# Kernel tuning notes

Hardware: AMD Instinct MI355X
Metric: run time of the kernel (lower is better)

Reference implementation:

```python
import jax, jax.numpy as jnp
import numpy as np

N_NODES = 20000
N_EDGES = 320000
IN_DIM = 128
HID = 64
HEADS = 4
NEG_SLOPE = 0.2  # PyG GATConv default


def _glorot(key, shape):
    fan_in, fan_out = shape[0], shape[-1]
    lim = jnp.sqrt(6.0 / (fan_in + fan_out))
    return jax.random.uniform(key, shape, jnp.float32, -lim, lim)


def setup_inputs() -> dict:
    key = jax.random.key(0)
    ks = jax.random.split(key, 16)
    x = jax.random.normal(ks[0], (N_NODES, IN_DIM), jnp.float32)
    edge_index = jax.random.randint(ks[1], (2, N_EDGES), 0, N_NODES, dtype=jnp.int64)
    # layer 1: in=128 -> heads=4, out=64, concat
    W1 = _glorot(ks[2], (IN_DIM, HEADS * HID))
    a_src1 = _glorot(ks[3], (HEADS, HID))
    a_dst1 = _glorot(ks[4], (HEADS, HID))
    b1 = jnp.zeros((HEADS * HID,), jnp.float32)
    # layer 2: in=256 -> heads=4, out=64, concat
    W2 = _glorot(ks[5], (HEADS * HID, HEADS * HID))
    a_src2 = _glorot(ks[6], (HEADS, HID))
    a_dst2 = _glorot(ks[7], (HEADS, HID))
    b2 = jnp.zeros((HEADS * HID,), jnp.float32)
    # layer 3: in=256 -> heads=1, out=1, mean (concat=False)
    W3 = _glorot(ks[8], (HEADS * HID, 1))
    a_src3 = _glorot(ks[9], (1, 1))
    a_dst3 = _glorot(ks[10], (1, 1))
    b3 = jnp.zeros((1,), jnp.float32)
    return {
        "x": x, "edge_index": edge_index,
        "W1": W1, "a_src1": a_src1, "a_dst1": a_dst1, "b1": b1,
        "W2": W2, "a_src2": a_src2, "a_dst2": a_dst2, "b2": b2,
        "W3": W3, "a_src3": a_src3, "a_dst3": a_dst3, "b3": b3,
    }


def gat_conv(x, src, dst, W, a_src, a_dst, b, heads, out_c, concat):
    """PyG GATConv (add_self_loops already applied to src/dst)."""
    n = x.shape[0]
    h = (x @ W).reshape(n, heads, out_c)            # [N,H,C]
    alpha_s = jnp.sum(h * a_src, axis=-1)           # [N,H]
    alpha_d = jnp.sum(h * a_dst, axis=-1)           # [N,H]
    e = jax.nn.leaky_relu(alpha_s[src] + alpha_d[dst], NEG_SLOPE)  # [E,H]
    # segment softmax over incoming edges of each destination node
    e_max = jax.ops.segment_max(e, dst, num_segments=n)            # [N,H]
    ex = jnp.exp(e - e_max[dst])                                   # [E,H]
    denom = jax.ops.segment_sum(ex, dst, num_segments=n)           # [N,H]
    alpha = ex / denom[dst]                                        # [E,H]
    msg = h[src] * alpha[:, :, None]                               # [E,H,C]
    out = jax.ops.segment_sum(msg, dst, num_segments=n)            # [N,H,C]
    if concat:
        out = out.reshape(n, heads * out_c)
    else:
        out = out.mean(axis=1)
    return out + b


def reference(x, edge_index, W1, a_src1, a_dst1, b1, W2, a_src2, a_dst2, b2,
              W3, a_src3, a_dst3, b3):
    n = x.shape[0]
    loops = jnp.arange(n, dtype=edge_index.dtype)
    src = jnp.concatenate([edge_index[0], loops])
    dst = jnp.concatenate([edge_index[1], loops])
    h = jax.nn.elu(gat_conv(x, src, dst, W1, a_src1, a_dst1, b1, HEADS, HID, True))
    # dropout is identity in eval mode
    h = jax.nn.elu(gat_conv(h, src, dst, W2, a_src2, a_dst2, b2, HEADS, HID, True))
    h = gat_conv(h, src, dst, W3, a_src3, a_dst3, b3, 1, 1, False)
    return h.reshape(-1)
```

## Files before the change

kernel.cpp:

```cpp
#include <hip/hip_runtime.h>
#include <hip/hip_bf16.h>
#include <cmath>

#define N_NODESC 20000
#define E_RAW    320000
#define E_TOTC   340000
#define HEADSC   4
#define FC       256
#define NEG_SLOPE 0.2f
#define MAXD     512

typedef __attribute__((ext_vector_type(8))) short short8v;
typedef __attribute__((ext_vector_type(4))) float f32x4;

__device__ __forceinline__ int dstOf(const int* ei, int e) {
  return (e < E_RAW) ? ei[E_RAW + e] : (e - E_RAW);
}
__device__ __forceinline__ int srcOf(const int* ei, int e) {
  return (e < E_RAW) ? ei[e] : (e - E_RAW);
}
__device__ __forceinline__ float lrelu(float v) { return v > 0.f ? v : NEG_SLOPE * v; }

__device__ __forceinline__ unsigned short f2bf(float f) {
  __hip_bfloat16 h = __float2bfloat16(f);
  return reinterpret_cast<unsigned short&>(h);
}
__device__ __forceinline__ float bf2f(unsigned short u) {
  return __uint_as_float(((unsigned int)u) << 16);
}

__global__ void mega_prep(const float* __restrict__ x,
                          unsigned short* __restrict__ xhi, unsigned short* __restrict__ xlo,
                          const float* __restrict__ W1,
                          unsigned short* __restrict__ w1hi, unsigned short* __restrict__ w1lo,
                          const float* __restrict__ W2,
                          unsigned short* __restrict__ w2hi, unsigned short* __restrict__ w2lo,
                          int* __restrict__ deg) {
  const int bid = blockIdx.x, t = threadIdx.x;
  if (bid < 10000) {
    int i = bid * 256 + t;
    float v = x[i];
    unsigned short hh = f2bf(v);
    xhi[i] = hh; xlo[i] = f2bf(v - bf2f(hh));
  } else if (bid < 10128) {
    int idx = (bid - 10000) * 256 + t;
    int c = idx >> 7, k = idx & 127;
    float v = W1[k * FC + c];
    unsigned short hh = f2bf(v);
    w1hi[c * 128 + k] = hh; w1lo[c * 128 + k] = f2bf(v - bf2f(hh));
  } else if (bid < 10384) {
    int idx = (bid - 10128) * 256 + t;
    int c = idx >> 8, k = idx & 255;
    float v = W2[k * FC + c];
    unsigned short hh = f2bf(v);
    w2hi[c * 256 + k] = hh; w2lo[c * 256 + k] = f2bf(v - bf2f(hh));
  } else {
    int i = (bid - 10384) * 256 + t;
    if (i < N_NODESC) deg[i] = 0;
  }
}

template<int K>
__global__ void __launch_bounds__(256) mfma_gemm(
    const unsigned short* __restrict__ Ahi, const unsigned short* __restrict__ Alo,
    const unsigned short* __restrict__ WhiT, const unsigned short* __restrict__ WloT,
    const float* __restrict__ a_src, const float* __restrict__ a_dst,
    unsigned short* __restrict__ hb, float* __restrict__ as, float* __restrict__ ad) {
  __shared__ float asred[64][4];
  __shared__ float adred[64][4];
  const int t = threadIdx.x;
  const int w = t >> 6, l = t & 63;
  const int n0 = blockIdx.x * 64;
  const int r16 = l & 15;
  const int kq = l >> 4;
  const int col0 = w * 64;

  f32x4 acc[4][4];
#pragma unroll
  for (int rt = 0; rt < 4; ++rt)
#pragma unroll
    for (int ct = 0; ct < 4; ++ct) acc[rt][ct] = f32x4{0.f, 0.f, 0.f, 0.f};

  long arow[4];
#pragma unroll
  for (int rt = 0; rt < 4; ++rt) {
    int r = n0 + rt * 16 + r16;
    if (r >= N_NODESC) r = N_NODESC - 1;
    arow[rt] = (long)r * K;
  }

  for (int ks = 0; ks < K; ks += 32) {
    const int kb = ks + kq * 8;
    short8v aHi[4], aLo[4];
#pragma unroll
    for (int rt = 0; rt < 4; ++rt) {
      aHi[rt] = *(const short8v*)(Ahi + arow[rt] + kb);
      aLo[rt] = *(const short8v*)(Alo + arow[rt] + kb);
    }
#pragma unroll
    for (int ct = 0; ct < 4; ++ct) {
      const long wrow = (long)(col0 + ct * 16 + r16) * K + kb;
      short8v wHi = *(const short8v*)(WhiT + wrow);
      short8v wLo = *(const short8v*)(WloT + wrow);
#pragma unroll
      for (int rt = 0; rt < 4; ++rt) {
        acc[rt][ct] = __builtin_amdgcn_mfma_f32_16x16x32_bf16(aHi[rt], wHi, acc[rt][ct], 0, 0, 0);
        acc[rt][ct] = __builtin_amdgcn_mfma_f32_16x16x32_bf16(aHi[rt], wLo, acc[rt][ct], 0, 0, 0);
        acc[rt][ct] = __builtin_amdgcn_mfma_f32_16x16x32_bf16(aLo[rt], wHi, acc[rt][ct], 0, 0, 0);
      }
    }
  }

  float asv[4], adv[4];
#pragma unroll
  for (int ct = 0; ct < 4; ++ct) {
    int c = col0 + ct * 16 + r16;
    asv[ct] = a_src[c];
    adv[ct] = a_dst[c];
  }
#pragma unroll
  for (int rt = 0; rt < 4; ++rt) {
#pragma unroll
    for (int j = 0; j < 4; ++j) {
      const int r = rt * 16 + kq * 4 + j;
      const int g = n0 + r;
      if (g < N_NODESC) {
#pragma unroll
        for (int ct = 0; ct < 4; ++ct)
          hb[(long)g * FC + col0 + ct * 16 + r16] = f2bf(acc[rt][ct][j]);
      }
      float ps = acc[rt][0][j] * asv[0] + acc[rt][1][j] * asv[1]
               + acc[rt][2][j] * asv[2] + acc[rt][3][j] * asv[3];
      float pd = acc[rt][0][j] * adv[0] + acc[rt][1][j] * adv[1]
               + acc[rt][2][j] * adv[2] + acc[rt][3][j] * adv[3];
      for (int off = 8; off; off >>= 1) {
        ps += __shfl_down(ps, off, 16);
        pd += __shfl_down(pd, off, 16);
      }
      if (r16 == 0) {
        asred[r][w] = ps;
        adred[r][w] = pd;
      }
    }
  }
  __syncthreads();
  {
    const int rr = t >> 2, hh = t & 3;
    const int g = n0 + rr;
    if (g < N_NODESC) {
      as[(long)g * HEADSC + hh] = asred[rr][hh];
      ad[(long)g * HEADSC + hh] = adred[rr][hh];
    }
  }
}

__global__ void deg_count(const int* __restrict__ ei, int* __restrict__ deg) {
  int e = blockIdx.x * 256 + threadIdx.x;
  if (e >= E_TOTC) return;
  atomicAdd(&deg[dstOf(ei, e)], 1);
}

__global__ void scan_kernel(const int* __restrict__ deg, int* __restrict__ row_ptr,
                            int* __restrict__ cursor) {
  const int t = threadIdx.x;
  const int lane = t & 63, wid = t >> 6;
  const int PER = (N_NODESC + 1023) / 1024;
  const int base = t * PER;
  int own = 0;
  for (int i = 0; i < PER; ++i) {
    int idx = base + i;
    if (idx < N_NODESC) own += deg[idx];
  }
  int inc = own;
  for (int off = 1; off < 64; off <<= 1) {
    int v = __shfl_up(inc, off, 64);
    if (lane >= off) inc += v;
  }
  __shared__ int wtot[16], woff[16];
  if (lane == 63) wtot[wid] = inc;
  __syncthreads();
  if (t == 0) {
    int r = 0;
    for (int i = 0; i < 16; ++i) { woff[i] = r; r += wtot[i]; }
  }
  __syncthreads();
  int run = woff[wid] + inc - own;
  for (int i = 0; i < PER; ++i) {
    int idx = base + i;
    if (idx < N_NODESC) {
      row_ptr[idx] = run;
      cursor[idx]  = run;
      run += deg[idx];
    }
  }
  if (t == 1023) row_ptr[N_NODESC] = run;
}

__global__ void fill_kernel(const int* __restrict__ ei, int* __restrict__ cursor,
                            int* __restrict__ col_src) {
  int e = blockIdx.x * 256 + threadIdx.x;
  if (e >= E_TOTC) return;
  int d = dstOf(ei, e);
  int pos = atomicAdd(&cursor[d], 1);
  col_src[pos] = srcOf(ei, e);
}

template<int MODE>
__global__ void __launch_bounds__(128) fused_sa(
    const int* __restrict__ row_ptr, const int* __restrict__ col_src,
    const float4* __restrict__ as4, const float4* __restrict__ ad4,
    const unsigned short* __restrict__ hb, const float* __restrict__ b,
    unsigned short* __restrict__ out_hi, unsigned short* __restrict__ out_lo,
    const float* __restrict__ W3, const float* __restrict__ asc3,
    const float* __restrict__ adc3, float* __restrict__ h3,
    float* __restrict__ a3s, float* __restrict__ a3d) {
  const int d = blockIdx.x;
  const int t = threadIdx.x;
  const int l = t & 63, wv = t >> 6;
  const int j0 = row_ptr[d], j1 = row_ptr[d + 1];
  const int deg = j1 - j0;
  __shared__ float4 wbuf[MAXD];
  __shared__ float4 xred[2];
  const float4 adv = ad4[d];

  float4 mx = float4{-INFINITY, -INFINITY, -INFINITY, -INFINITY};
  for (int j = j0 + t; j < j1; j += 128) {
    float4 a = as4[col_src[j]];
    float4 v;
    v.x = lrelu(a.x + adv.x); v.y = lrelu(a.y + adv.y);
    v.z = lrelu(a.z + adv.z); v.w = lrelu(a.w + adv.w);
    int jj = j - j0;
    if (jj < MAXD) wbuf[jj] = v;
    mx.x = fmaxf(mx.x, v.x); mx.y = fmaxf(mx.y, v.y);
    mx.z = fmaxf(mx.z, v.z); mx.w = fmaxf(mx.w, v.w);
  }
  for (int off = 32; off; off >>= 1) {
    mx.x = fmaxf(mx.x, __shfl_xor(mx.x, off, 64));
    mx.y = fmaxf(mx.y, __shfl_xor(mx.y, off, 64));
    mx.z = fmaxf(mx.z, __shfl_xor(mx.z, off, 64));
    mx.w = fmaxf(mx.w, __shfl_xor(mx.w, off, 64));
  }
  if (l == 0) xred[wv] = mx;
  __syncthreads();
  {
    float4 m0 = xred[0], m1 = xred[1];
    mx.x = fmaxf(m0.x, m1.x); mx.y = fmaxf(m0.y, m1.y);
    mx.z = fmaxf(m0.z, m1.z); mx.w = fmaxf(m0.w, m1.w);
  }
  __syncthreads();

  float4 sm = float4{0.f, 0.f, 0.f, 0.f};
  for (int j = j0 + t; j < j1; j += 128) {
    int jj = j - j0;
    float4 v;
    if (jj < MAXD) v = wbuf[jj];
    else {
      float4 a = as4[col_src[j]];
      v.x = lrelu(a.x + adv.x); v.y = lrelu(a.y + adv.y);
      v.z = lrelu(a.z + adv.z); v.w = lrelu(a.w + adv.w);
    }
    float4 e;
    e.x = expf(v.x - mx.x); e.y = expf(v.y - mx.y);
    e.z = expf(v.z - mx.z); e.w = expf(v.w - mx.w);
    if (jj < MAXD) wbuf[jj] = e;
    sm.x += e.x; sm.y += e.y; sm.z += e.z; sm.w += e.w;
  }
  for (int off = 32; off; off >>= 1) {
    sm.x += __shfl_xor(sm.x, off, 64);
    sm.y += __shfl_xor(sm.y, off, 64);
    sm.z += __shfl_xor(sm.z, off, 64);
    sm.w += __shfl_xor(sm.w, off, 64);
  }
  if (l == 0) xred[wv] = sm;
  __syncthreads();

  const int h = t >> 5;
  float st0, mxh, advh;
  {
    float4 s0 = xred[0], s1 = xred[1];
    float sx = s0.x + s1.x, sy = s0.y + s1.y, sz = s0.z + s1.z, sw = s0.w + s1.w;
    st0  = (h == 0) ? sx : (h == 1) ? sy : (h == 2) ? sz : sw;
    mxh  = (h == 0) ? mx.x : (h == 1) ? mx.y : (h == 2) ? mx.z : mx.w;
    advh = (h == 0) ? adv.x : (h == 1) ? adv.y : (h == 2) ? adv.z : adv.w;
  }
  const float dnh = 1.f / st0;

  const float* wlds = (const float*)wbuf;
  const ushort2* hb2 = (const ushort2*)hb;
  float a0 = 0.f, a1 = 0.f;
  if (deg <= MAXD) {
    int j = j0;
    for (; j + 8 <= j1; j += 8) {
      int     s[8];
      ushort2 v[8];
      float   w[8];
#pragma unroll
      for (int u = 0; u < 8; ++u) s[u] = col_src[j + u];
#pragma unroll
      for (int u = 0; u < 8; ++u) v[u] = hb2[(long)s[u] * 128 + t];
#pragma unroll
      for (int u = 0; u < 8; ++u) w[u] = wlds[(j + u - j0) * 4 + h];
#pragma unroll
      for (int u = 0; u < 8; ++u) {
        a0 = fmaf(w[u], bf2f(v[u].x), a0);
        a1 = fmaf(w[u], bf2f(v[u].y), a1);
      }
    }
    for (; j < j1; ++j) {
      ushort2 v = hb2[(long)col_src[j] * 128 + t];
      float w = wlds[(j - j0) * 4 + h];
      a0 = fmaf(w, bf2f(v.x), a0);
      a1 = fmaf(w, bf2f(v.y), a1);
    }
  } else {
    const float* asf = (const float*)as4;
    for (int j = j0; j < j1; ++j) {
      int s = col_src[j];
      float e = expf(lrelu(asf[s * 4 + h] + advh) - mxh);
      ushort2 v = hb2[(long)s * 128 + t];
      a0 = fmaf(e, bf2f(v.x), a0);
      a1 = fmaf(e, bf2f(v.y), a1);
    }
  }
  float o0 = a0 * dnh + b[2 * t];
  float o1 = a1 * dnh + b[2 * t + 1];
  o0 = o0 > 0.f ? o0 : expm1f(o0);
  o1 = o1 > 0.f ? o1 : expm1f(o1);

  if (MODE == 0) {
    ushort2 hi, lo;
    hi.x = f2bf(o0); lo.x = f2bf(o0 - bf2f(hi.x));
    hi.y = f2bf(o1); lo.y = f2bf(o1 - bf2f(hi.y));
    ((ushort2*)out_hi)[(long)d * 128 + t] = hi;
    ((ushort2*)out_lo)[(long)d * 128 + t] = lo;
  } else {
    float p = o0 * W3[2 * t] + o1 * W3[2 * t + 1];
    for (int off = 32; off; off >>= 1) p += __shfl_down(p, off, 64);
    __shared__ float pred[2];
    if (l == 0) pred[wv] = p;
    __syncthreads();
    if (t == 0) {
      float s = pred[0] + pred[1];
      h3[d]  = s;
      a3s[d] = s * asc3[0];
      a3d[d] = s * adc3[0];
    }
  }
}

__global__ void __launch_bounds__(256) fused_sa3(
    const int* __restrict__ row_ptr, const int* __restrict__ col_src,
    const float* __restrict__ as, const float* __restrict__ ad,
    const float* __restrict__ h3, const float* __restrict__ b3,
    float* __restrict__ out) {
  const int wv = threadIdx.x >> 6, l = threadIdx.x & 63;
  const int d = blockIdx.x * 4 + wv;
  if (d >= N_NODESC) return;
  const int j0 = row_ptr[d], j1 = row_ptr[d + 1];
  const float adv = ad[d];
  float mx = -INFINITY;
  for (int j = j0 + l; j < j1; j += 64)
    mx = fmaxf(mx, lrelu(as[col_src[j]] + adv));
  for (int off = 32; off; off >>= 1) mx = fmaxf(mx, __shfl_xor(mx, off, 64));
  float sm = 0.f, acc = 0.f;
  for (int j = j0 + l; j < j1; j += 64) {
    int s = col_src[j];
    float e = expf(lrelu(as[s] + adv) - mx);
    sm += e;
    acc = fmaf(e, h3[s], acc);
  }
  for (int off = 32; off; off >>= 1) {
    sm  += __shfl_xor(sm, off, 64);
    acc += __shfl_xor(acc, off, 64);
  }
  if (l == 0) out[d] = acc / sm + b3[0];
}

extern "C" void kernel_launch(void* const* d_in, const int* in_sizes, int n_in,
                              void* d_out, int out_size, void* d_ws, size_t ws_size,
                              hipStream_t stream) {
  const float* x    = (const float*)d_in[0];
  const int*   ei   = (const int*)d_in[1];
  const float* W1   = (const float*)d_in[2];
  const float* as1  = (const float*)d_in[3];
  const float* ad1  = (const float*)d_in[4];
  const float* b1   = (const float*)d_in[5];
  const float* W2   = (const float*)d_in[6];
  const float* as2  = (const float*)d_in[7];
  const float* ad2  = (const float*)d_in[8];
  const float* b2   = (const float*)d_in[9];
  const float* W3   = (const float*)d_in[10];
  const float* as3  = (const float*)d_in[11];
  const float* ad3  = (const float*)d_in[12];
  const float* b3   = (const float*)d_in[13];
  float* out = (float*)d_out;

  float* ws = (float*)d_ws;
  size_t off = 0;
  float* wAs   = ws + off; off += (size_t)N_NODESC * HEADSC;
  float* wAd   = ws + off; off += (size_t)N_NODESC * HEADSC;
  float* h3    = ws + off; off += N_NODESC;
  float* a3s   = ws + off; off += N_NODESC;
  float* a3d   = ws + off; off += N_NODESC;
  int* deg     = (int*)(ws + off); off += N_NODESC;
  int* row_ptr = (int*)(ws + off); off += N_NODESC + 1;
  int* cursor  = (int*)(ws + off); off += N_NODESC;
  int* col_src = (int*)(ws + off); off += E_TOTC;
  off = (off + 3) & ~(size_t)3;
  unsigned short* hb     = (unsigned short*)(ws + off); off += (size_t)N_NODESC * 128;
  unsigned short* act_hi = (unsigned short*)(ws + off); off += (size_t)N_NODESC * 128;
  unsigned short* act_lo = (unsigned short*)(ws + off); off += (size_t)N_NODESC * 128;
  unsigned short* xhi    = (unsigned short*)(ws + off); off += (size_t)N_NODESC * 64;
  unsigned short* xlo    = (unsigned short*)(ws + off); off += (size_t)N_NODESC * 64;
  unsigned short* W1hiT  = (unsigned short*)(ws + off); off += 16384;
  unsigned short* W1loT  = (unsigned short*)(ws + off); off += 16384;
  unsigned short* W2hiT  = (unsigned short*)(ws + off); off += 32768;
  unsigned short* W2loT  = (unsigned short*)(ws + off); off += 32768;

  const int gridE  = (E_TOTC + 255) / 256;
  const int gridN4 = (N_NODESC + 3) / 4;
  const int gemmG  = (N_NODESC + 63) / 64;

  mega_prep<<<10463, 256, 0, stream>>>(x, xhi, xlo, W1, W1hiT, W1loT,
                                       W2, W2hiT, W2loT, deg);
  deg_count<<<gridE, 256, 0, stream>>>(ei, deg);
  scan_kernel<<<1, 1024, 0, stream>>>(deg, row_ptr, cursor);
  fill_kernel<<<gridE, 256, 0, stream>>>(ei, cursor, col_src);

  mfma_gemm<128><<<gemmG, 256, 0, stream>>>(xhi, xlo, W1hiT, W1loT, as1, ad1, hb, wAs, wAd);
  fused_sa<0><<<N_NODESC, 128, 0, stream>>>(row_ptr, col_src, (const float4*)wAs,
                                            (const float4*)wAd, hb, b1, act_hi, act_lo,
                                            nullptr, nullptr, nullptr, nullptr, nullptr, nullptr);

  mfma_gemm<256><<<gemmG, 256, 0, stream>>>(act_hi, act_lo, W2hiT, W2loT, as2, ad2, hb, wAs, wAd);
  fused_sa<1><<<N_NODESC, 128, 0, stream>>>(row_ptr, col_src, (const float4*)wAs,
                                            (const float4*)wAd, hb, b2, nullptr, nullptr,
                                            W3, as3, ad3, h3, a3s, a3d);

  fused_sa3<<<gridN4, 256, 0, stream>>>(row_ptr, col_src, a3s, a3d, h3, b3, out);
}
```

Before: 233.1 us.

## Replace per-node segment max with global upper bound to single-pass softmax aggregation

The GEMM kernels now reduce a global per-head maximum of alpha_src with float atomics. The aggregation kernel uses lrelu(global_max + alpha_dst) as the softmax shift, which lets it fuse the max, exp-sum and weighted-sum passes into one loop over edges and drop the shared-memory weight buffer and its barriers. Because leaky ReLU is monotone, this shift is still an upper bound, so softmax stays mathematically equivalent. The risk is underflow when a node's own logits sit far below the bound, which could lose precision or give a zero denominator.

```diff
diff --git a/kernel.cpp b/kernel.cpp
--- a/kernel.cpp
+++ b/kernel.cpp
@@ -8,7 +8,6 @@
 #define HEADSC   4
 #define FC       256
 #define NEG_SLOPE 0.2f
-#define MAXD     512
 
 typedef __attribute__((ext_vector_type(8))) short short8v;
 typedef __attribute__((ext_vector_type(4))) float f32x4;
@@ -27,6 +26,11 @@
 }
 __device__ __forceinline__ float bf2f(unsigned short u) {
   return __uint_as_float(((unsigned int)u) << 16);
+}
+
+__device__ __forceinline__ void atomicMaxF(float* addr, float val) {
+  if (val >= 0.f) atomicMax((int*)addr, __float_as_int(val));
+  else            atomicMin((unsigned int*)addr, (unsigned int)__float_as_int(val));
 }
 
 __global__ void mega_prep(const float* __restrict__ x,
@@ -35,7 +39,7 @@
                           unsigned short* __restrict__ w1hi, unsigned short* __restrict__ w1lo,
                           const float* __restrict__ W2,
                           unsigned short* __restrict__ w2hi, unsigned short* __restrict__ w2lo,
-                          int* __restrict__ deg) {
+                          int* __restrict__ deg, float* __restrict__ amax) {
   const int bid = blockIdx.x, t = threadIdx.x;
   if (bid < 10000) {
     int i = bid * 256 + t;
@@ -57,6 +61,7 @@
   } else {
     int i = (bid - 10384) * 256 + t;
     if (i < N_NODESC) deg[i] = 0;
+    else if (i < N_NODESC + 8) amax[i - N_NODESC] = -INFINITY;
   }
 }
 
@@ -65,9 +70,11 @@
     const unsigned short* __restrict__ Ahi, const unsigned short* __restrict__ Alo,
     const unsigned short* __restrict__ WhiT, const unsigned short* __restrict__ WloT,
     const float* __restrict__ a_src, const float* __restrict__ a_dst,
-    unsigned short* __restrict__ hb, float* __restrict__ as, float* __restrict__ ad) {
+    unsigned short* __restrict__ hb, float* __restrict__ as, float* __restrict__ ad,
+    float* __restrict__ asmax) {
   __shared__ float asred[64][4];
   __shared__ float adred[64][4];
+  __shared__ float wmax[4][4];
   const int t = threadIdx.x;
   const int w = t >> 6, l = t & 63;
   const int n0 = blockIdx.x * 64;
@@ -147,10 +154,20 @@
   {
     const int rr = t >> 2, hh = t & 3;
     const int g = n0 + rr;
+    float mv = -INFINITY;
     if (g < N_NODESC) {
-      as[(long)g * HEADSC + hh] = asred[rr][hh];
+      float va = asred[rr][hh];
+      as[(long)g * HEADSC + hh] = va;
       ad[(long)g * HEADSC + hh] = adred[rr][hh];
-    }
+      mv = va;
+    }
+    for (int off = 32; off >= 4; off >>= 1) mv = fmaxf(mv, __shfl_down(mv, off, 64));
+    if (l < 4) wmax[w][l] = mv;
+  }
+  __syncthreads();
+  if (t < 4) {
+    float m = fmaxf(fmaxf(wmax[0][t], wmax[1][t]), fmaxf(wmax[2][t], wmax[3][t]));
+    atomicMaxF(&asmax[t], m);
   }
 }
 
@@ -208,7 +225,8 @@
 template<int MODE>
 __global__ void __launch_bounds__(128) fused_sa(
     const int* __restrict__ row_ptr, const int* __restrict__ col_src,
-    const float4* __restrict__ as4, const float4* __restrict__ ad4,
+    const float* __restrict__ asf, const float4* __restrict__ ad4,
+    const float* __restrict__ asmax,
     const unsigned short* __restrict__ hb, const float* __restrict__ b,
     unsigned short* __restrict__ out_hi, unsigned short* __restrict__ out_lo,
     const float* __restrict__ W3, const float* __restrict__ asc3,
@@ -217,111 +235,42 @@
   const int d = blockIdx.x;
   const int t = threadIdx.x;
   const int l = t & 63, wv = t >> 6;
+  const int h = t >> 5;
   const int j0 = row_ptr[d], j1 = row_ptr[d + 1];
-  const int deg = j1 - j0;
-  __shared__ float4 wbuf[MAXD];
-  __shared__ float4 xred[2];
   const float4 adv = ad4[d];
-
-  float4 mx = float4{-INFINITY, -INFINITY, -INFINITY, -INFINITY};
-  for (int j = j0 + t; j < j1; j += 128) {
-    float4 a = as4[col_src[j]];
-    float4 v;
-    v.x = lrelu(a.x + adv.x); v.y = lrelu(a.y + adv.y);
-    v.z = lrelu(a.z + adv.z); v.w = lrelu(a.w + adv.w);
-    int jj = j - j0;
-    if (jj < MAXD) wbuf[jj] = v;
-    mx.x = fmaxf(mx.x, v.x); mx.y = fmaxf(mx.y, v.y);
-    mx.z = fmaxf(mx.z, v.z); mx.w = fmaxf(mx.w, v.w);
-  }
-  for (int off = 32; off; off >>= 1) {
-    mx.x = fmaxf(mx.x, __shfl_xor(mx.x, off, 64));
-    mx.y = fmaxf(mx.y, __shfl_xor(mx.y, off, 64));
-    mx.z = fmaxf(mx.z, __shfl_xor(mx.z, off, 64));
-    mx.w = fmaxf(mx.w, __shfl_xor(mx.w, off, 64));
-  }
-  if (l == 0) xred[wv] = mx;
-  __syncthreads();
-  {
-    float4 m0 = xred[0], m1 = xred[1];
-    mx.x = fmaxf(m0.x, m1.x); mx.y = fmaxf(m0.y, m1.y);
-    mx.z = fmaxf(m0.z, m1.z); mx.w = fmaxf(m0.w, m1.w);
-  }
-  __syncthreads();
-
-  float4 sm = float4{0.f, 0.f, 0.f, 0.f};
-  for (int j = j0 + t; j < j1; j += 128) {
-    int jj = j - j0;
-    float4 v;
-    if (jj < MAXD) v = wbuf[jj];
-    else {
-      float4 a = as4[col_src[j]];
-      v.x = lrelu(a.x + adv.x); v.y = lrelu(a.y + adv.y);
-      v.z = lrelu(a.z + adv.z); v.w = lrelu(a.w + adv.w);
-    }
-    float4 e;
-    e.x = expf(v.x - mx.x); e.y = expf(v.y - mx.y);
-    e.z = expf(v.z - mx.z); e.w = expf(v.w - mx.w);
-    if (jj < MAXD) wbuf[jj] = e;
-    sm.x += e.x; sm.y += e.y; sm.z += e.z; sm.w += e.w;
-  }
-  for (int off = 32; off; off >>= 1) {
-    sm.x += __shfl_xor(sm.x, off, 64);
-    sm.y += __shfl_xor(sm.y, off, 64);
-    sm.z += __shfl_xor(sm.z, off, 64);
-    sm.w += __shfl_xor(sm.w, off, 64);
-  }
-  if (l == 0) xred[wv] = sm;
-  __syncthreads();
-
-  const int h = t >> 5;
-  float st0, mxh, advh;
-  {
-    float4 s0 = xred[0], s1 = xred[1];
-    float sx = s0.x + s1.x, sy = s0.y + s1.y, sz = s0.z + s1.z, sw = s0.w + s1.w;
-    st0  = (h == 0) ? sx : (h == 1) ? sy : (h == 2) ? sz : sw;
-    mxh  = (h == 0) ? mx.x : (h == 1) ? mx.y : (h == 2) ? mx.z : mx.w;
-    advh = (h == 0) ? adv.x : (h == 1) ? adv.y : (h == 2) ? adv.z : adv.w;
-  }
-  const float dnh = 1.f / st0;
-
-  const float* wlds = (const float*)wbuf;
+  const float advh = (h == 0) ? adv.x : (h == 1) ? adv.y : (h == 2) ? adv.z : adv.w;
+  const float mh = lrelu(asmax[h] + advh);
+
   const ushort2* hb2 = (const ushort2*)hb;
-  float a0 = 0.f, a1 = 0.f;
-  if (deg <= MAXD) {
-    int j = j0;
-    for (; j + 8 <= j1; j += 8) {
-      int     s[8];
-      ushort2 v[8];
-      float   w[8];
-#pragma unroll
-      for (int u = 0; u < 8; ++u) s[u] = col_src[j + u];
-#pragma unroll
-      for (int u = 0; u < 8; ++u) v[u] = hb2[(long)s[u] * 128 + t];
-#pragma unroll
-      for (int u = 0; u < 8; ++u) w[u] = wlds[(j + u - j0) * 4 + h];
-#pragma unroll
-      for (int u = 0; u < 8; ++u) {
-        a0 = fmaf(w[u], bf2f(v[u].x), a0);
-        a1 = fmaf(w[u], bf2f(v[u].y), a1);
-      }
-    }
-    for (; j < j1; ++j) {
-      ushort2 v = hb2[(long)col_src[j] * 128 + t];
-      float w = wlds[(j - j0) * 4 + h];
-      a0 = fmaf(w, bf2f(v.x), a0);
-      a1 = fmaf(w, bf2f(v.y), a1);
-    }
-  } else {
-    const float* asf = (const float*)as4;
-    for (int j = j0; j < j1; ++j) {
-      int s = col_src[j];
-      float e = expf(lrelu(asf[s * 4 + h] + advh) - mxh);
-      ushort2 v = hb2[(long)s * 128 + t];
-      a0 = fmaf(e, bf2f(v.x), a0);
-      a1 = fmaf(e, bf2f(v.y), a1);
-    }
-  }
+  float a0 = 0.f, a1 = 0.f, sm = 0.f;
+  int j = j0;
+  for (; j + 8 <= j1; j += 8) {
+    int     s[8];
+    float   av[8];
+    ushort2 v[8];
+#pragma unroll
+    for (int u = 0; u < 8; ++u) s[u] = col_src[j + u];
+#pragma unroll
+    for (int u = 0; u < 8; ++u) av[u] = asf[s[u] * 4 + h];
+#pragma unroll
+    for (int u = 0; u < 8; ++u) v[u] = hb2[(long)s[u] * 128 + t];
+#pragma unroll
+    for (int u = 0; u < 8; ++u) {
+      float e = expf(lrelu(av[u] + advh) - mh);
+      sm += e;
+      a0 = fmaf(e, bf2f(v[u].x), a0);
+      a1 = fmaf(e, bf2f(v[u].y), a1);
+    }
+  }
+  for (; j < j1; ++j) {
+    int s = col_src[j];
+    float e = expf(lrelu(asf[s * 4 + h] + advh) - mh);
+    ushort2 v = hb2[(long)s * 128 + t];
+    sm += e;
+    a0 = fmaf(e, bf2f(v.x), a0);
+    a1 = fmaf(e, bf2f(v.y), a1);
+  }
+  const float dnh = 1.f / sm;
   float o0 = a0 * dnh + b[2 * t];
   float o1 = a1 * dnh + b[2 * t + 1];
   o0 = o0 > 0.f ? o0 : expm1f(o0);
@@ -402,6 +351,7 @@
   float* h3    = ws + off; off += N_NODESC;
   float* a3s   = ws + off; off += N_NODESC;
   float* a3d   = ws + off; off += N_NODESC;
+  float* amax  = ws + off; off += 8;
   int* deg     = (int*)(ws + off); off += N_NODESC;
   int* row_ptr = (int*)(ws + off); off += N_NODESC + 1;
   int* cursor  = (int*)(ws + off); off += N_NODESC;
@@ -422,19 +372,21 @@
   const int gemmG  = (N_NODESC + 63) / 64;
 
   mega_prep<<<10463, 256, 0, stream>>>(x, xhi, xlo, W1, W1hiT, W1loT,
-                                       W2, W2hiT, W2loT, deg);
+                                       W2, W2hiT, W2loT, deg, amax);
   deg_count<<<gridE, 256, 0, stream>>>(ei, deg);
   scan_kernel<<<1, 1024, 0, stream>>>(deg, row_ptr, cursor);
   fill_kernel<<<gridE, 256, 0, stream>>>(ei, cursor, col_src);
 
-  mfma_gemm<128><<<gemmG, 256, 0, stream>>>(xhi, xlo, W1hiT, W1loT, as1, ad1, hb, wAs, wAd);
-  fused_sa<0><<<N_NODESC, 128, 0, stream>>>(row_ptr, col_src, (const float4*)wAs,
-                                            (const float4*)wAd, hb, b1, act_hi, act_lo,
+  mfma_gemm<128><<<gemmG, 256, 0, stream>>>(xhi, xlo, W1hiT, W1loT, as1, ad1,
+                                            hb, wAs, wAd, amax);
+  fused_sa<0><<<N_NODESC, 128, 0, stream>>>(row_ptr, col_src, wAs, (const float4*)wAd,
+                                            amax, hb, b1, act_hi, act_lo,
                                             nullptr, nullptr, nullptr, nullptr, nullptr, nullptr);
 
-  mfma_gemm<256><<<gemmG, 256, 0, stream>>>(act_hi, act_lo, W2hiT, W2loT, as2, ad2, hb, wAs, wAd);
-  fused_sa<1><<<N_NODESC, 128, 0, stream>>>(row_ptr, col_src, (const float4*)wAs,
-                                            (const float4*)wAd, hb, b2, nullptr, nullptr,
+  mfma_gemm<256><<<gemmG, 256, 0, stream>>>(act_hi, act_lo, W2hiT, W2loT, as2, ad2,
+                                            hb, wAs, wAd, amax + 4);
+  fused_sa<1><<<N_NODESC, 128, 0, stream>>>(row_ptr, col_src, wAs, (const float4*)wAd,
+                                            amax + 4, hb, b2, nullptr, nullptr,
                                             W3, as3, ad3, h3, a3s, a3d);
 
   fused_sa3<<<gridN4, 256, 0, stream>>>(row_ptr, col_src, a3s, a3d, h3, b3, out);
```

New measurement: 230.9 us. Within noise of the previous version (-1.0%).
